# Performance work log

Hardware: AMD Instinct MI355X
Metric: run time of the kernel (lower is better)

## Reference

```python
import jax, jax.numpy as jnp
import numpy as np

B, S, D = 64, 4096, 256
LN_EPS = 1e-3  # Keras LayerNormalization default epsilon


def setup_inputs() -> dict:
    key = jax.random.key(0)
    k1, k2, k3 = jax.random.split(key, 3)
    x = jax.random.normal(k1, (B, S, D), dtype=jnp.float32)
    mask = jnp.ones((B, S), dtype=jnp.float32)
    gamma = jnp.ones((D,), dtype=jnp.float32)       # LayerNorm scale
    beta = jnp.zeros((D,), dtype=jnp.float32)       # LayerNorm offset
    w = jax.random.normal(k2, (D,), dtype=jnp.float32) * (1.0 / np.sqrt(D))  # Dense(1) kernel
    b = jnp.zeros((), dtype=jnp.float32)            # Dense(1) bias
    return {"x": x, "mask": mask, "gamma": gamma, "beta": beta, "w": w, "b": b}


def reference(x, mask, gamma, beta, w, b):
    # LayerNorm over feature dim
    mu = jnp.mean(x, axis=-1, keepdims=True)
    var = jnp.mean(jnp.square(x - mu), axis=-1, keepdims=True)
    xn = (x - mu) * jax.lax.rsqrt(var + LN_EPS) * gamma + beta  # [B,S,D]
    # Dense(1) score projection
    score = jnp.einsum('bsd,d->bs', xn, w) + b                  # [B,S]
    # Mask out padded positions, softmax over sequence axis
    score = score + (1.0 - mask) * -1e9
    weights = jax.nn.softmax(score, axis=1)                     # [B,S]
    # Weighted sum over sequence
    return jnp.einsum('bsd,bs->bd', x, weights)                 # [B,D]
```

## Files before the change

kernel.cpp:

```cpp
#include <hip/hip_runtime.h>
#include <math.h>

#define B_   64
#define S_   4096
#define D_   256
#define CH   32
#define ROWS_PER_CHUNK (S_ / CH)
#define NWAVE 4
#define RPW   8
#define ROWS_PER_BLOCK_ITER (NWAVE * RPW)
#define NITER (ROWS_PER_CHUNK / ROWS_PER_BLOCK_ITER)
#define LN_EPS 1e-3f

typedef float f4 __attribute__((ext_vector_type(4)));

__global__ __launch_bounds__(256) void pool_pass1(
    const float* __restrict__ x, const float* __restrict__ mask,
    const float* __restrict__ gamma, const float* __restrict__ w,
    float* __restrict__ ws_acc, float* __restrict__ ws_m, float* __restrict__ ws_l)
{
    const int blk   = blockIdx.x;
    const int b     = blk / CH;
    const int chunk = blk % CH;
    const int tid   = threadIdx.x;
    const int lane  = tid & 63;
    const int wave  = tid >> 6;
    const int o     = lane >> 3;
    const int t     = lane & 7;

    f4 gw[8];
    float sgw = 0.0f;
    #pragma unroll
    for (int k = 0; k < 8; ++k) {
        const int d = t * 4 + 32 * k;
        const f4 g4 = *(const f4*)(gamma + d);
        const f4 w4 = *(const f4*)(w + d);
        gw[k] = g4 * w4;
        sgw += gw[k][0] + gw[k][1] + gw[k][2] + gw[k][3];
    }
    #pragma unroll
    for (int off = 4; off > 0; off >>= 1) sgw += __shfl_xor(sgw, off, 64);

    const int row0 = chunk * ROWS_PER_CHUNK + wave * RPW + o;
    const float* xbase = x + ((size_t)b * S_ + row0) * D_ + t * 4;
    const float* mbase = mask + (size_t)b * S_ + row0;

    float m = -3.0e38f;
    float l = 0.0f;
    f4 acc[8];
    #pragma unroll
    for (int k = 0; k < 8; ++k) acc[k] = (f4)0.0f;

    f4 v[8];
    #pragma unroll
    for (int k = 0; k < 8; ++k)
        v[k] = *(const f4*)(xbase + 32 * k);
    float msk = mbase[0];

    for (int i = 0; i < NITER; ++i) {
        const int inx = (i + 1 < NITER) ? i + 1 : i;
        f4 vn[8];
        #pragma unroll
        for (int k = 0; k < 8; ++k)
            vn[k] = *(const f4*)(xbase + (size_t)inx * ROWS_PER_BLOCK_ITER * D_ + 32 * k);
        const float mskn = mbase[inx * ROWS_PER_BLOCK_ITER];

        float s1 = 0.f, s2 = 0.f, s3 = 0.f;
        #pragma unroll
        for (int k = 0; k < 8; ++k) {
            #pragma unroll
            for (int j = 0; j < 4; ++j) {
                const float e = v[k][j];
                s1 += e;
                s2 += e * e;
                s3 += e * gw[k][j];
            }
        }
        #pragma unroll
        for (int off = 4; off > 0; off >>= 1) {
            s1 += __shfl_xor(s1, off, 64);
            s2 += __shfl_xor(s2, off, 64);
            s3 += __shfl_xor(s3, off, 64);
        }
        const float mu    = s1 * (1.0f / D_);
        const float var   = s2 * (1.0f / D_) - mu * mu;
        const float rstd  = rsqrtf(var + LN_EPS);
        const float score = rstd * (s3 - mu * sgw) + (1.0f - msk) * -1e9f;

        const float mnew  = fmaxf(m, score);
        const float scale = __expf(m - mnew);
        const float p     = __expf(score - mnew);
        m = mnew;
        l = l * scale + p;
        #pragma unroll
        for (int k = 0; k < 8; ++k) acc[k] = acc[k] * scale + p * v[k];

        #pragma unroll
        for (int k = 0; k < 8; ++k) v[k] = vn[k];
        msk = mskn;
    }

    __shared__ float s_acc[ROWS_PER_BLOCK_ITER][D_];
    __shared__ float s_m[ROWS_PER_BLOCK_ITER];
    __shared__ float s_l[ROWS_PER_BLOCK_ITER];
    const int g = wave * RPW + o;
    #pragma unroll
    for (int k = 0; k < 8; ++k) *(f4*)&s_acc[g][t * 4 + 32 * k] = acc[k];
    if (t == 0) { s_m[g] = m; s_l[g] = l; }
    __syncthreads();

    float M = -3.0e38f;
    #pragma unroll
    for (int gg = 0; gg < ROWS_PER_BLOCK_ITER; ++gg) M = fmaxf(M, s_m[gg]);
    float L = 0.f, a = 0.f;
    #pragma unroll
    for (int gg = 0; gg < ROWS_PER_BLOCK_ITER; ++gg) {
        const float e = __expf(s_m[gg] - M);
        L += e * s_l[gg];
        a += e * s_acc[gg][tid];
    }
    ws_acc[(size_t)blk * D_ + tid] = a;
    if (tid == 0) { ws_m[blk] = M; ws_l[blk] = L; }
}

__global__ __launch_bounds__(256) void pool_pass2(
    const float* __restrict__ ws_acc, const float* __restrict__ ws_m,
    const float* __restrict__ ws_l, float* __restrict__ out)
{
    const int b = blockIdx.x;
    const int d = threadIdx.x;

    float M = -3.0e38f;
    #pragma unroll
    for (int c = 0; c < CH; ++c) M = fmaxf(M, ws_m[b * CH + c]);

    float L = 0.0f, a = 0.0f;
    #pragma unroll
    for (int c = 0; c < CH; ++c) {
        const float e = __expf(ws_m[b * CH + c] - M);
        L += e * ws_l[b * CH + c];
        a += e * ws_acc[((size_t)(b * CH + c)) * D_ + d];
    }
    out[(size_t)b * D_ + d] = a / L;
}

extern "C" void kernel_launch(void* const* d_in, const int* in_sizes, int n_in,
                              void* d_out, int out_size, void* d_ws, size_t ws_size,
                              hipStream_t stream) {
    const float* x     = (const float*)d_in[0];
    const float* mask  = (const float*)d_in[1];
    const float* gamma = (const float*)d_in[2];
    const float* w     = (const float*)d_in[4];
    float* out = (float*)d_out;

    float* ws_acc = (float*)d_ws;
    float* ws_m   = ws_acc + (size_t)B_ * CH * D_;
    float* ws_l   = ws_m + B_ * CH;

    pool_pass1<<<B_ * CH, 256, 0, stream>>>(x, mask, gamma, w, ws_acc, ws_m, ws_l);
    pool_pass2<<<B_, 256, 0, stream>>>(ws_acc, ws_m, ws_l, out);
}
```

Baseline: 368.5 us.

## Use 16 lanes per row with triple-buffered nontemporal prefetch and preloaded mask

```diff
diff --git a/kernel.cpp b/kernel.cpp
--- a/kernel.cpp
+++ b/kernel.cpp
@@ -7,8 +7,7 @@
 #define CH   32
 #define ROWS_PER_CHUNK (S_ / CH)
 #define NWAVE 4
-#define RPW   8
-#define ROWS_PER_BLOCK_ITER (NWAVE * RPW)
+#define ROWS_PER_BLOCK_ITER (NWAVE * 4)
 #define NITER (ROWS_PER_CHUNK / ROWS_PER_BLOCK_ITER)
 #define LN_EPS 1e-3f
 
@@ -25,49 +24,58 @@
     const int tid   = threadIdx.x;
     const int lane  = tid & 63;
     const int wave  = tid >> 6;
-    const int o     = lane >> 3;
-    const int t     = lane & 7;
+    const int q     = lane >> 4;
+    const int t     = lane & 15;
 
-    f4 gw[8];
+    f4 gw[4];
     float sgw = 0.0f;
     #pragma unroll
-    for (int k = 0; k < 8; ++k) {
-        const int d = t * 4 + 32 * k;
+    for (int k = 0; k < 4; ++k) {
+        const int d = t * 4 + 64 * k;
         const f4 g4 = *(const f4*)(gamma + d);
         const f4 w4 = *(const f4*)(w + d);
         gw[k] = g4 * w4;
         sgw += gw[k][0] + gw[k][1] + gw[k][2] + gw[k][3];
     }
     #pragma unroll
-    for (int off = 4; off > 0; off >>= 1) sgw += __shfl_xor(sgw, off, 64);
+    for (int off = 8; off > 0; off >>= 1) sgw += __shfl_xor(sgw, off, 64);
 
-    const int row0 = chunk * ROWS_PER_CHUNK + wave * RPW + o;
+    const int row0 = chunk * ROWS_PER_CHUNK + wave * 4 + q;
     const float* xbase = x + ((size_t)b * S_ + row0) * D_ + t * 4;
     const float* mbase = mask + (size_t)b * S_ + row0;
 
+    float mk[NITER];
+    #pragma unroll
+    for (int i = 0; i < NITER; ++i)
+        mk[i] = mbase[i * ROWS_PER_BLOCK_ITER];
+
     float m = -3.0e38f;
     float l = 0.0f;
-    f4 acc[8];
+    f4 acc[4];
     #pragma unroll
-    for (int k = 0; k < 8; ++k) acc[k] = (f4)0.0f;
+    for (int k = 0; k < 4; ++k) acc[k] = (f4)0.0f;
 
-    f4 v[8];
+    f4 buf[3][4];
     #pragma unroll
-    for (int k = 0; k < 8; ++k)
-        v[k] = *(const f4*)(xbase + 32 * k);
-    float msk = mbase[0];
+    for (int s = 0; s < 2; ++s)
+        #pragma unroll
+        for (int k = 0; k < 4; ++k)
+            buf[s][k] = __builtin_nontemporal_load(
+                (const f4*)(xbase + (size_t)s * ROWS_PER_BLOCK_ITER * D_ + 64 * k));
 
+    #pragma unroll
     for (int i = 0; i < NITER; ++i) {
-        const int inx = (i + 1 < NITER) ? i + 1 : i;
-        f4 vn[8];
+        const int ipf = (i + 2 < NITER) ? i + 2 : NITER - 1;
         #pragma unroll
-        for (int k = 0; k < 8; ++k)
-            vn[k] = *(const f4*)(xbase + (size_t)inx * ROWS_PER_BLOCK_ITER * D_ + 32 * k);
-        const float mskn = mbase[inx * ROWS_PER_BLOCK_ITER];
+        for (int k = 0; k < 4; ++k)
+            buf[(i + 2) % 3][k] = __builtin_nontemporal_load(
+                (const f4*)(xbase + (size_t)ipf * ROWS_PER_BLOCK_ITER * D_ + 64 * k));
+
+        const f4* v = buf[i % 3];
 
         float s1 = 0.f, s2 = 0.f, s3 = 0.f;
         #pragma unroll
-        for (int k = 0; k < 8; ++k) {
+        for (int k = 0; k < 4; ++k) {
             #pragma unroll
             for (int j = 0; j < 4; ++j) {
                 const float e = v[k][j];
@@ -77,7 +85,7 @@
             }
         }
         #pragma unroll
-        for (int off = 4; off > 0; off >>= 1) {
+        for (int off = 8; off > 0; off >>= 1) {
             s1 += __shfl_xor(s1, off, 64);
             s2 += __shfl_xor(s2, off, 64);
             s3 += __shfl_xor(s3, off, 64);
@@ -85,7 +93,7 @@
         const float mu    = s1 * (1.0f / D_);
         const float var   = s2 * (1.0f / D_) - mu * mu;
         const float rstd  = rsqrtf(var + LN_EPS);
-        const float score = rstd * (s3 - mu * sgw) + (1.0f - msk) * -1e9f;
+        const float score = rstd * (s3 - mu * sgw) + (1.0f - mk[i]) * -1e9f;
 
         const float mnew  = fmaxf(m, score);
         const float scale = __expf(m - mnew);
@@ -93,19 +101,15 @@
         m = mnew;
         l = l * scale + p;
         #pragma unroll
-        for (int k = 0; k < 8; ++k) acc[k] = acc[k] * scale + p * v[k];
-
-        #pragma unroll
-        for (int k = 0; k < 8; ++k) v[k] = vn[k];
-        msk = mskn;
+        for (int k = 0; k < 4; ++k) acc[k] = acc[k] * scale + p * v[k];
     }
 
     __shared__ float s_acc[ROWS_PER_BLOCK_ITER][D_];
     __shared__ float s_m[ROWS_PER_BLOCK_ITER];
     __shared__ float s_l[ROWS_PER_BLOCK_ITER];
-    const int g = wave * RPW + o;
+    const int g = wave * 4 + q;
     #pragma unroll
-    for (int k = 0; k < 8; ++k) *(f4*)&s_acc[g][t * 4 + 32 * k] = acc[k];
+    for (int k = 0; k < 4; ++k) *(f4*)&s_acc[g][t * 4 + 64 * k] = acc[k];
     if (t == 0) { s_m[g] = m; s_l[g] = l; }
     __syncthreads();
 
```

Measured after the change: 345.0 us (median of 2 runs). -6.4%, faster.
